# Performance work log

Measured on AMD Instinct MI355X. Metric: run time of the kernel, lower is better.

The kernel has to match this reference:

```python
import jax, jax.numpy as jnp
import numpy as np
from jax import lax

SCALE = 2
UP_K = 5  # reassembly kernel
ENC_K = 3


def conv2d(x, w, padding):
    # x: (N,C,H,W), w: (O,I,kh,kw)
    return lax.conv_general_dilated(
        x, w, window_strides=(1, 1), padding=[(padding, padding)] * 2,
        dimension_numbers=("NCHW", "OIHW", "NCHW"))


def pixel_shuffle(x, r):
    # (N, C*r*r, H, W) -> (N, C, r*H, r*W), matching torch.nn.functional.pixel_shuffle
    N, Crr, H, W = x.shape
    C = Crr // (r * r)
    x = x.reshape(N, C, r, r, H, W)
    x = x.transpose(0, 1, 4, 2, 5, 3)  # N, C, H, r, W, r
    return x.reshape(N, C, H * r, W * r)


def setup_inputs() -> dict:
    key = jax.random.key(0)
    k1, k2, k3, k4 = jax.random.split(key, 4)
    N, C, H, W = 2, 256, 64, 64
    comp = 64
    enc_out = UP_K * UP_K * SCALE * SCALE  # 100
    features = jax.random.normal(k1, (N, C, H, W), dtype=jnp.float32)
    w_comp = jax.random.normal(k2, (comp, C, 1, 1), dtype=jnp.float32) * (1.0 / np.sqrt(C))
    b_comp = jax.random.normal(k3, (comp,), dtype=jnp.float32) * 0.01
    w_enc = jax.random.normal(k4, (enc_out, comp, ENC_K, ENC_K), dtype=jnp.float32) * 0.001
    return {"features": features, "w_comp": w_comp, "b_comp": b_comp, "w_enc": w_enc}


def carafe_forward(features, w_comp, b_comp, w_enc):
    N, C, H, W = features.shape
    r = SCALE
    # 1) channel compression (1x1 conv + bias; norm_type=None)
    compressed = conv2d(features, w_comp, padding=0) + b_comp[None, :, None, None]
    # 2) content encoding -> (N, k^2 * r^2, H, W)
    kp = conv2d(compressed, w_enc, padding=(ENC_K - 1) // 2)
    # pixel shuffle -> (N, k^2, rH, rW)
    kp = pixel_shuffle(kp, r)
    # 3) softmax over the k^2 kernel dim
    kernels = jax.nn.softmax(kp, axis=1)  # (N, k2, sH, sW)
    # 4) nearest-neighbor upsample
    feat_up = jnp.repeat(jnp.repeat(features, r, axis=2), r, axis=3)  # (N,C,sH,sW)
    sH, sW = H * r, W * r
    pad = (UP_K // 2) * r  # unfold padding, dilation = r
    xpad = jnp.pad(feat_up, ((0, 0), (0, 0), (pad, pad), (pad, pad)))
    # accumulate the softmax-weighted gather over the k x k dilated neighborhood
    out = jnp.zeros((N, C, sH, sW), dtype=features.dtype)
    for i in range(UP_K):
        for j in range(UP_K):
            patch = xpad[:, :, i * r:i * r + sH, j * r:j * r + sW]  # (N,C,sH,sW)
            wgt = kernels[:, i * UP_K + j]  # (N,sH,sW)
            out = out + patch * wgt[:, None, :, :]
    return out


def reference(features, w_comp, b_comp, w_enc):
    return carafe_forward(features, w_comp, b_comp, w_enc)
```

## Files before the change

kernel.cpp:

```cpp
#include <hip/hip_runtime.h>
#include <hip/hip_bf16.h>
#include <math.h>

#define CIN 256

typedef __attribute__((ext_vector_type(8))) short short8v;
typedef __attribute__((ext_vector_type(4))) float f32x4;


__device__ inline ushort f2bf(float x) {
    __hip_bfloat16 b = __float2bfloat16(x);
    return *reinterpret_cast<ushort*>(&b);
}

__device__ inline float dpp_shl1(float x) {
    int r = __builtin_amdgcn_update_dpp(0, __builtin_bit_cast(int, x), 0x130, 0xf, 0xf, true);
    return __builtin_bit_cast(float, r);
}
__device__ inline float dpp_shr1(float x) {
    int r = __builtin_amdgcn_update_dpp(0, __builtin_bit_cast(int, x), 0x138, 0xf, 0xf, true);
    return __builtin_bit_cast(float, r);
}

__global__ __launch_bounds__(256) void prep_compress(const float* __restrict__ w_comp,
                                                     const float* __restrict__ w_enc,
                                                     const float* __restrict__ b_comp,
                                                     const float* __restrict__ feat,
                                                     ushort* __restrict__ Bsw,
                                                     ushort* __restrict__ compB) {
    int bid = blockIdx.x, tid = threadIdx.x;
    if (bid >= 256) {
        int i = (bid - 256) * 256 + tid;
        int j = i & 7, lane = (i >> 3) & 63, rest = i >> 9;
        int nf = rest & 7, ks = rest >> 3;
        int ct = ks >> 1, dh = ct / 3, dw = ct % 3;
        int cc = (ks & 1) * 32 + (lane >> 4) * 8 + j;
        int o  = nf * 16 + (lane & 15);
        float v = (o < 100) ? w_enc[((o * 64 + cc) * 3 + dh) * 3 + dw] : 0.f;
        Bsw[i] = f2bf(v);
        return;
    }
    __shared__ ushort at[32][264];
    int p0 = bid * 32;
    int n = p0 >> 12, hw0 = p0 & 4095;
    const float* fb = feat + (size_t)n * CIN * 4096 + hw0;
    {
        int p4 = tid & 7, cr = tid >> 3;
        #pragma unroll
        for (int k = 0; k < 8; ++k) {
            int c = cr + k * 32;
            float4 v = *reinterpret_cast<const float4*>(fb + (size_t)c * 4096 + p4 * 4);
            at[p4 * 4 + 0][c] = f2bf(v.x);
            at[p4 * 4 + 1][c] = f2bf(v.y);
            at[p4 * 4 + 2][c] = f2bf(v.z);
            at[p4 * 4 + 3][c] = f2bf(v.w);
        }
    }
    __syncthreads();
    int lane = tid & 63, nf = tid >> 6;
    int lr = lane & 15, lk = lane >> 4;
    int cc = nf * 16 + lr;
    f32x4 acc0 = {0, 0, 0, 0}, acc1 = {0, 0, 0, 0};
    const float* wrow = w_comp + (size_t)cc * 256;
    #pragma unroll
    for (int ks = 0; ks < 8; ++ks) {
        float4 b0 = *reinterpret_cast<const float4*>(wrow + ks * 32 + lk * 8);
        float4 b1 = *reinterpret_cast<const float4*>(wrow + ks * 32 + lk * 8 + 4);
        short8v b;
        b[0] = (short)f2bf(b0.x); b[1] = (short)f2bf(b0.y);
        b[2] = (short)f2bf(b0.z); b[3] = (short)f2bf(b0.w);
        b[4] = (short)f2bf(b1.x); b[5] = (short)f2bf(b1.y);
        b[6] = (short)f2bf(b1.z); b[7] = (short)f2bf(b1.w);
        short8v a0 = *reinterpret_cast<const short8v*>(&at[lr][ks * 32 + lk * 8]);
        short8v a1 = *reinterpret_cast<const short8v*>(&at[16 + lr][ks * 32 + lk * 8]);
        acc0 = __builtin_amdgcn_mfma_f32_16x16x32_bf16(a0, b, acc0, 0, 0, 0);
        acc1 = __builtin_amdgcn_mfma_f32_16x16x32_bf16(a1, b, acc1, 0, 0, 0);
    }
    float bv = b_comp[cc];
    #pragma unroll
    for (int i = 0; i < 4; ++i) {
        compB[(size_t)(p0 + lk * 4 + i) * 64 + cc]      = f2bf(acc0[i] + bv);
        compB[(size_t)(p0 + 16 + lk * 4 + i) * 64 + cc] = f2bf(acc1[i] + bv);
    }
}

__global__ __launch_bounds__(512) void enc_gemm_softmax(const ushort* __restrict__ compB,
                                                        const ushort* __restrict__ Bsw,
                                                        float* __restrict__ wgt) {
    int p0 = blockIdx.x * 16;
    int n = p0 >> 12, h = (p0 >> 6) & 63, w0 = p0 & 63;
    int tid = threadIdx.x, lane = tid & 63, nf = tid >> 6;
    int lr = lane & 15, lk = lane >> 4;
    int wpix = w0 + lr;
    f32x4 acc = {0, 0, 0, 0};
    #pragma unroll
    for (int ks = 0; ks < 18; ++ks) {
        int ct = ks >> 1, dh = ct / 3, dw = ct - dh * 3;
        int hh = h + dh - 1;
        if ((unsigned)hh >= 64u) continue;
        int ww = wpix + dw - 1;
        short8v a = {};
        if ((unsigned)ww < 64u)
            a = *reinterpret_cast<const short8v*>(
                    compB + ((size_t)(n * 4096 + hh * 64 + ww) * 64 + (ks & 1) * 32 + lk * 8));
        short8v b = *reinterpret_cast<const short8v*>(
                    Bsw + ((size_t)(ks * 8 + nf) * 64 + lane) * 8);
        acc = __builtin_amdgcn_mfma_f32_16x16x32_bf16(a, b, acc, 0, 0, 0);
    }
    __shared__ float kp_lds[16][132];
    #pragma unroll
    for (int i = 0; i < 4; ++i)
        kp_lds[lk * 4 + i][nf * 16 + lr] = acc[i];
    __syncthreads();
    if (tid < 64) {
        int pl = tid & 15, sub = tid >> 4;
        float v[25], mx = -1e30f;
        #pragma unroll
        for (int t = 0; t < 25; ++t) { v[t] = kp_lds[pl][t * 4 + sub]; mx = fmaxf(mx, v[t]); }
        float s = 0.f;
        #pragma unroll
        for (int t = 0; t < 25; ++t) { v[t] = expf(v[t] - mx); s += v[t]; }
        float inv = 1.f / s;
        float* o = wgt + ((size_t)((n * 64 + h) * 4 + sub)) * 1600 + (w0 + pl);
        #pragma unroll
        for (int t = 0; t < 25; ++t) o[t * 64] = v[t] * inv;
    }
}

__global__ __launch_bounds__(256, 4) void apply_v3(const float* __restrict__ feat,
                                                   const float* __restrict__ wgt,
                                                   float* __restrict__ out) {
    int bid = blockIdx.x;
    int wgid = (bid & 7) * 128 + (bid >> 3);
    int cg = wgid & 7;
    int nh = wgid >> 3;
    int n = nh >> 6, h = nh & 63;
    int tid = threadIdx.x;
    int w  = tid & 63;
    int ci = tid >> 6;
    int c0 = cg * 32 + ci * 8;

    __shared__ float wlds[4 * 25 * 64];
    {
        const float* wg = wgt + (size_t)nh * 6400;
        #pragma unroll
        for (int it = 0; it < 25; ++it)
            wlds[it * 256 + tid] = wg[it * 256 + tid];
    }
    __syncthreads();

    const float* fbase = feat + ((size_t)(n * CIN + c0)) * 4096;

    float acc[4][8];
    #pragma unroll
    for (int s = 0; s < 4; ++s)
        #pragma unroll
        for (int k = 0; k < 8; ++k) acc[s][k] = 0.f;

    #pragma unroll
    for (int i = 0; i < 5; ++i) {
        int hh = h + i - 2;
        if ((unsigned)hh >= 64u) continue;
        float wv[4][5];
        #pragma unroll
        for (int s = 0; s < 4; ++s)
            #pragma unroll
            for (int j = 0; j < 5; ++j)
                wv[s][j] = wlds[(s * 25 + i * 5 + j) * 64 + w];
        #pragma unroll
        for (int k = 0; k < 8; ++k) {
            float v = fbase[(size_t)k * 4096 + (hh << 6) + w];
            float vm1 = dpp_shr1(v);
            float vm2 = dpp_shr1(vm1);
            float vp1 = dpp_shl1(v);
            float vp2 = dpp_shl1(vp1);
            float fv[5] = {vm2, vm1, v, vp1, vp2};
            #pragma unroll
            for (int j = 0; j < 5; ++j)
                #pragma unroll
                for (int s = 0; s < 4; ++s)
                    acc[s][k] += fv[j] * wv[s][j];
        }
    }

    #pragma unroll
    for (int k = 0; k < 8; ++k) {
        float* o = out + ((size_t)(n * CIN + c0 + k) * 128 + 2 * h) * 128 + 2 * w;
        *reinterpret_cast<float2*>(o)       = make_float2(acc[0][k], acc[1][k]);
        *reinterpret_cast<float2*>(o + 128) = make_float2(acc[2][k], acc[3][k]);
    }
}

extern "C" void kernel_launch(void* const* d_in, const int* in_sizes, int n_in,
                              void* d_out, int out_size, void* d_ws, size_t ws_size,
                              hipStream_t stream) {
    const float* features = (const float*)d_in[0];
    const float* w_comp   = (const float*)d_in[1];
    const float* b_comp   = (const float*)d_in[2];
    const float* w_enc    = (const float*)d_in[3];
    float* out = (float*)d_out;
    float* ws  = (float*)d_ws;

    ushort* Bsw   = (ushort*)ws;
    ushort* compB = (ushort*)(ws + 36864);
    float*  wgt   = ws + 299008;

    hipLaunchKernelGGL(prep_compress, dim3(544), dim3(256), 0, stream,
                       w_comp, w_enc, b_comp, features, Bsw, compB);
    hipLaunchKernelGGL(enc_gemm_softmax, dim3(512), dim3(512), 0, stream, compB, Bsw, wgt);
    hipLaunchKernelGGL(apply_v3, dim3(1024), dim3(256), 0, stream, features, wgt, out);
}
```

Before: 35.98 us.

## Double-buffer feature row loads and transpose weight LDS layout for vector reads

The apply kernel now prefetches the next input row's 8 channel values into registers while computing the current row, using clamped row offsets and a validity flag in place of an early continue. The softmax weights are also re-laid out in LDS as [row][w][tap][subpixel], so each lane reads its four subpixel weights with one 16-byte load instead of 20 scalar reads. The aim is to hide global load latency and cut LDS instructions. In exchange it uses more registers, adds index arithmetic and LDS write conflicts in the staging loop, and issues loads for boundary rows that are then discarded.

```diff
diff --git a/kernel.cpp b/kernel.cpp
--- a/kernel.cpp
+++ b/kernel.cpp
@@ -127,7 +127,7 @@
     }
 }
 
-__global__ __launch_bounds__(256, 4) void apply_v3(const float* __restrict__ feat,
+__global__ __launch_bounds__(256, 4) void apply_v4(const float* __restrict__ feat,
                                                    const float* __restrict__ wgt,
                                                    float* __restrict__ out) {
     int bid = blockIdx.x;
@@ -140,12 +140,19 @@
     int ci = tid >> 6;
     int c0 = cg * 32 + ci * 8;
 
-    __shared__ float wlds[4 * 25 * 64];
+    __shared__ float wlds[6400];
     {
         const float* wg = wgt + (size_t)nh * 6400;
         #pragma unroll
-        for (int it = 0; it < 25; ++it)
-            wlds[it * 256 + tid] = wg[it * 256 + tid];
+        for (int it = 0; it < 25; ++it) {
+            int idx = it * 256 + tid;
+            float v = wg[idx];
+            int s  = idx / 1600;
+            int r  = idx - s * 1600;
+            int t  = r >> 6, ww = r & 63;
+            int i_ = t / 5, j_ = t - i_ * 5;
+            wlds[((i_ * 64 + ww) * 5 + j_) * 4 + s] = v;
+        }
     }
     __syncthreads();
 
@@ -157,29 +164,48 @@
         #pragma unroll
         for (int k = 0; k < 8; ++k) acc[s][k] = 0.f;
 
+    int   rofs[5];
+    bool  rok[5];
     #pragma unroll
     for (int i = 0; i < 5; ++i) {
         int hh = h + i - 2;
-        if ((unsigned)hh >= 64u) continue;
-        float wv[4][5];
-        #pragma unroll
-        for (int s = 0; s < 4; ++s)
+        rok[i]  = (unsigned)hh < 64u;
+        int hc  = hh < 0 ? 0 : (hh > 63 ? 63 : hh);
+        rofs[i] = (hc << 6) + w;
+    }
+
+    float La[8], Lb[8];
+    #pragma unroll
+    for (int k = 0; k < 8; ++k) La[k] = fbase[(size_t)k * 4096 + rofs[0]];
+
+    #pragma unroll
+    for (int i = 0; i < 5; ++i) {
+        float* Lc = (i & 1) ? Lb : La;
+        float* Ln = (i & 1) ? La : Lb;
+        if (i < 4) {
+            #pragma unroll
+            for (int k = 0; k < 8; ++k) Ln[k] = fbase[(size_t)k * 4096 + rofs[i + 1]];
+        }
+        if (rok[i]) {
+            f32x4 wv[5];
             #pragma unroll
             for (int j = 0; j < 5; ++j)
-                wv[s][j] = wlds[(s * 25 + i * 5 + j) * 64 + w];
-        #pragma unroll
-        for (int k = 0; k < 8; ++k) {
-            float v = fbase[(size_t)k * 4096 + (hh << 6) + w];
-            float vm1 = dpp_shr1(v);
-            float vm2 = dpp_shr1(vm1);
-            float vp1 = dpp_shl1(v);
-            float vp2 = dpp_shl1(vp1);
-            float fv[5] = {vm2, vm1, v, vp1, vp2};
+                wv[j] = *reinterpret_cast<const f32x4*>(&wlds[((i * 64 + w) * 5 + j) * 4]);
             #pragma unroll
-            for (int j = 0; j < 5; ++j)
+            for (int k = 0; k < 8; ++k) {
+                float v = Lc[k];
+                float vm1 = dpp_shr1(v);
+                float vm2 = dpp_shr1(vm1);
+                float vp1 = dpp_shl1(v);
+                float vp2 = dpp_shl1(vp1);
+                float fv[5] = {vm2, vm1, v, vp1, vp2};
                 #pragma unroll
-                for (int s = 0; s < 4; ++s)
-                    acc[s][k] += fv[j] * wv[s][j];
+                for (int j = 0; j < 5; ++j) {
+                    #pragma unroll
+                    for (int s = 0; s < 4; ++s)
+                        acc[s][k] += fv[j] * wv[j][s];
+                }
+            }
         }
     }
 
@@ -208,5 +234,5 @@
     hipLaunchKernelGGL(prep_compress, dim3(544), dim3(256), 0, stream,
                        w_comp, w_enc, b_comp, features, Bsw, compB);
     hipLaunchKernelGGL(enc_gemm_softmax, dim3(512), dim3(512), 0, stream, compB, Bsw, wgt);
-    hipLaunchKernelGGL(apply_v3, dim3(1024), dim3(256), 0, stream, features, wgt, out);
-}
+    hipLaunchKernelGGL(apply_v4, dim3(1024), dim3(256), 0, stream, features, wgt, out);
+}
```

Result: slower. 37.35 us (+3.8%).
